# Performance work log

Measured on AMD Instinct MI355X. Metric: run time of the kernel, lower is better.

The kernel has to match this reference:

```python
import jax, jax.numpy as jnp
import numpy as np

D = 384      # d_model
DM = 256     # memory feature dim
DF = 1536    # dim_feedforward
EPS = 1e-5


def _layer_norm(x, g, b):
    m = jnp.mean(x, axis=-1, keepdims=True)
    v = jnp.mean(jnp.square(x - m), axis=-1, keepdims=True)
    return (x - m) * jax.lax.rsqrt(v + EPS) * g + b


def setup_inputs() -> dict:
    key = jax.random.key(0)
    ks = jax.random.split(key, 24)
    B, T, T1, Tc = 8, 2048, 2048, 2048
    s = 0.02
    inp = {
        "tgt": jax.random.normal(ks[0], (B, T, D), jnp.float32),
        "memory": jax.random.normal(ks[1], (B, T1, DM), jnp.float32),
        "a1": jnp.float32(0.5),
        "score_c": jax.random.normal(ks[2], (B, 1, Tc, T1), jnp.float32) * 0.1,
        "out_c": jax.random.normal(ks[3], (B, Tc, D), jnp.float32),
        # attention projections
        "Wq": jax.random.normal(ks[4], (D, D), jnp.float32) * s,
        "bq": jnp.zeros((D,), jnp.float32),
        "Wk": jax.random.normal(ks[5], (DM, D), jnp.float32) * s,
        "bk": jnp.zeros((D,), jnp.float32),
        "Wv": jax.random.normal(ks[6], (DM, D), jnp.float32) * s,
        "bv": jnp.zeros((D,), jnp.float32),
        "Wu": jax.random.normal(ks[7], (D, D), jnp.float32) * s,  # unknown
        "bu": jnp.zeros((D,), jnp.float32),
        "Wn": jax.random.normal(ks[8], (D, D), jnp.float32) * s,  # known
        "bn": jnp.zeros((D,), jnp.float32),
        # FFN
        "W1": jax.random.normal(ks[9], (D, DF), jnp.float32) * s,
        "b1": jnp.zeros((DF,), jnp.float32),
        "W2": jax.random.normal(ks[10], (DF, D), jnp.float32) * s,
        "b2": jnp.zeros((D,), jnp.float32),
        # LayerNorms
        "g1": jnp.ones((D,), jnp.float32),
        "be1": jnp.zeros((D,), jnp.float32),
        "g2": jnp.ones((D,), jnp.float32),
        "be2": jnp.zeros((D,), jnp.float32),
    }
    return inp


def reference(tgt, memory, a1, score_c, out_c,
              Wq, bq, Wk, bk, Wv, bv, Wu, bu, Wn, bn,
              W1, b1, W2, b2, g1, be1, g2, be2):
    # --- En_De_Attention (n_head = 1; dropout p=0 / eval mode -> identity) ---
    scale = 1.0 / jnp.sqrt(jnp.float32(D))
    q = tgt @ Wq + bq                  # [B,T,D]
    k = memory @ Wk + bk               # [B,T1,D]
    v = memory @ Wv + bv               # [B,T1,D]
    att = jnp.einsum('btd,bsd->bts', q, k) * scale            # [B,T,T1]

    unknow = tgt @ Wu + bu             # [B,T,D]
    know = out_c @ Wn + bn             # [B,Tc,D]
    score1 = jnp.einsum('btd,bcd->btc', unknow, know) * scale  # [B,T,Tc]
    mixed = jnp.einsum('btc,bcs->bts', score1, score_c[:, 0])  # [B,T,T1]

    # tt = a1 in (0,1]: blended-score branch of the original module
    score = a1 * jax.nn.softmax(mixed, axis=-1) \
          + (1.0 - a1) * jax.nn.softmax(att, axis=-1)          # [B,T,T1]
    z = jnp.einsum('bts,bsd->btd', score, v)                   # [B,T,D]

    # --- residual + norm1 ---
    x = _layer_norm(tgt + z, g1, be1)
    # --- FFN (relu) + residual + norm2 (dropout eval -> identity) ---
    ff = jax.nn.relu(x @ W1 + b1) @ W2 + b2
    out = _layer_norm(x + ff, g2, be2)
    # score2 returned with head dim, matching torch shape [B,1,T,T1]
    return out, score[:, None]
```

## Files before the change

### kernel.cpp

```cpp
#include <hip/hip_runtime.h>
#include <stdint.h>

typedef __attribute__((ext_vector_type(8))) short bf16x8;
typedef __attribute__((ext_vector_type(4))) float f32x4;

__device__ __forceinline__ short f2bf(float f) {
    union { float f; unsigned u; } v; v.f = f;
    unsigned r = v.u + 0x7fffu + ((v.u >> 16) & 1u);
    return (short)(r >> 16);
}
__device__ __forceinline__ float bf2f(short s) {
    union { unsigned u; float f; } v;
    v.u = ((unsigned)(unsigned short)s) << 16;
    return v.f;
}

__device__ __forceinline__ void gld16(const void* g, void* l) {
    auto gp = reinterpret_cast<const __attribute__((address_space(1))) unsigned int*>(
        reinterpret_cast<uintptr_t>(g));
    auto lp = reinterpret_cast<__attribute__((address_space(3))) unsigned int*>(
        reinterpret_cast<uintptr_t>(l));
    __builtin_amdgcn_global_load_lds(gp, lp, 16, 0, 0);
}

template<int OUTBF, int BIASMODE , int DORELU>
__global__ __launch_bounds__(256, 2) void gemm128p(
    const short* __restrict__ Ag, const short* __restrict__ Bg,
    void* __restrict__ Cg, const float* __restrict__ bias,
    int K, int N, long long sA, long long sB, long long sC, float scale)
{
    __shared__ short lds[2 * 16384];
    const int t = threadIdx.x;
    const int lane = t & 63;
    const int wave = t >> 6;
    const int wm = wave >> 1, wn = wave & 1;

    const int gx = gridDim.x, gy = gridDim.y;
    const int nwg = gx * gy * gridDim.z;
    int id = blockIdx.x + gx * (blockIdx.y + gy * blockIdx.z);
    id = (id & 7) * (nwg >> 3) + (id >> 3);
    const int bx = id % gx;
    const int by = (id / gx) % gy;
    const int bz = id / (gx * gy);

    const long long row0 = (long long)by * 128;
    const long long col0 = (long long)bx * 128;
    const int NT = K >> 6;

    const int srow = t >> 3;
    const int gk = ((t & 7) ^ (srow & 7)) * 8;
    const short* Asrc = Ag + (long long)bz * sA + (row0 + srow) * (long long)K + gk;
    const short* Bsrc = Bg + (long long)bz * sB + (col0 + srow) * (long long)K + gk;

    const int frow = lane & 15;
    const int fq = lane >> 4;

    f32x4 acc[4][4] = {};

#define STAGE_A(WB, KC) do { _Pragma("unroll") \
        for (int r = 0; r < 4; ++r) \
            gld16(Asrc + (KC) + (long long)r * 32 * K, &lds[(WB) + t * 8 + r * 2048]); } while (0)
#define STAGE_B(WB, KC) do { _Pragma("unroll") \
        for (int r = 0; r < 4; ++r) \
            gld16(Bsrc + (KC) + (long long)r * 32 * K, &lds[(WB) + 8192 + t * 8 + r * 2048]); } while (0)

#define RD_A(RB, M, KS) (*(const bf16x8*)&lds[(RB) + (wm * 64 + (M) * 16 + frow) * 64 + \
        ((((KS) << 2) | fq) ^ (frow & 7)) * 8])
#define RD_B(RB, Nn, KS) (*(const bf16x8*)&lds[(RB) + 8192 + (wn * 64 + (Nn) * 16 + frow) * 64 + \
        ((((KS) << 2) | fq) ^ (frow & 7)) * 8])

    STAGE_A(0, 0);
    STAGE_B(0, 0);
    asm volatile("s_waitcnt vmcnt(0)\ns_barrier" ::: "memory");

    for (int kt = 0; kt < NT; ++kt) {
        const int rb = (kt & 1) << 14;
        const int wb = ((kt + 1) & 1) << 14;
        const bool st = (kt + 1) < NT;
        const long long kc = (long long)(kt + 1) << 6;

        bf16x8 av[4], bv[4];

#pragma unroll
        for (int m = 0; m < 4; ++m) av[m] = RD_A(rb, m, 0);
#pragma unroll
        for (int n = 0; n < 4; ++n) bv[n] = RD_B(rb, n, 0);
        if (st) STAGE_A(wb, kc);
        asm volatile("s_barrier" ::: "memory");
        __builtin_amdgcn_s_setprio(1);
#pragma unroll
        for (int m = 0; m < 4; ++m)
#pragma unroll
            for (int n = 0; n < 4; ++n)
                acc[m][n] = __builtin_amdgcn_mfma_f32_16x16x32_bf16(av[m], bv[n], acc[m][n], 0, 0, 0);
        __builtin_amdgcn_s_setprio(0);
        asm volatile("s_barrier" ::: "memory");

#pragma unroll
        for (int m = 0; m < 4; ++m) av[m] = RD_A(rb, m, 1);
#pragma unroll
        for (int n = 0; n < 4; ++n) bv[n] = RD_B(rb, n, 1);
        if (st) STAGE_B(wb, kc);
        asm volatile("s_barrier" ::: "memory");
        __builtin_amdgcn_s_setprio(1);
#pragma unroll
        for (int m = 0; m < 4; ++m)
#pragma unroll
            for (int n = 0; n < 4; ++n)
                acc[m][n] = __builtin_amdgcn_mfma_f32_16x16x32_bf16(av[m], bv[n], acc[m][n], 0, 0, 0);
        __builtin_amdgcn_s_setprio(0);
        if (st) asm volatile("s_waitcnt vmcnt(0)\ns_barrier" ::: "memory");
        else    asm volatile("s_barrier" ::: "memory");
    }
#undef STAGE_A
#undef STAGE_B
#undef RD_A
#undef RD_B

    const int crow = (lane >> 4) * 4;
    const int ccol = lane & 15;
    const long long cz = (long long)bz * sC;
#pragma unroll
    for (int m = 0; m < 4; ++m)
#pragma unroll
        for (int n = 0; n < 4; ++n)
#pragma unroll
            for (int i = 0; i < 4; ++i) {
                long long r = row0 + wm * 64 + m * 16 + crow + i;
                long long c = col0 + wn * 64 + n * 16 + ccol;
                float v = acc[m][n][i] * scale;
                if (BIASMODE == 1) v += bias[c];
                if (BIASMODE == 2) v += bias[r];
                if (DORELU) v = fmaxf(v, 0.0f);
                long long idx = cz + r * (long long)N + c;
                if (OUTBF) ((short*)Cg)[idx] = f2bf(v);
                else ((float*)Cg)[idx] = v;
            }
}

__global__ __launch_bounds__(256) void cast_kernel(
    const float* __restrict__ in, short* __restrict__ out, long long n)
{
    long long i = ((long long)blockIdx.x * 256 + threadIdx.x) * 4;
    if (i + 3 < n) {
        float4 v = *(const float4*)&in[i];
        short4 o;
        o.x = f2bf(v.x); o.y = f2bf(v.y); o.z = f2bf(v.z); o.w = f2bf(v.w);
        *(short4*)&out[i] = o;
    }
}

__global__ __launch_bounds__(256) void transpose_cast(
    const float* __restrict__ in, short* __restrict__ out,
    int R, int C, long long sIn, long long sOut)
{
    __shared__ float tile[64][65];
    const long long zi = (long long)blockIdx.z * sIn;
    const long long zo = (long long)blockIdx.z * sOut;
    const int r0 = blockIdx.y * 64, c0 = blockIdx.x * 64;
    const int lr = threadIdx.x >> 6, lc = threadIdx.x & 63;
#pragma unroll
    for (int i = 0; i < 16; ++i) {
        int r = lr * 16 + i;
        tile[r][lc] = in[zi + (long long)(r0 + r) * C + c0 + lc];
    }
    __syncthreads();
#pragma unroll
    for (int i = 0; i < 16; ++i) {
        int r = lr * 16 + i;
        out[zo + (long long)(c0 + r) * R + r0 + lc] = f2bf(tile[lc][r]);
    }
}

__global__ __launch_bounds__(256) void softmax_blend(
    const short* __restrict__ attb, const short* __restrict__ mixb,
    const float* __restrict__ a1p,
    float* __restrict__ outF, short* __restrict__ outB)
{
    const int S = 2048;
    const long long row = blockIdx.x;
    const short* ar = attb + row * S;
    const short* mr = mixb + row * S;
    const int t = threadIdx.x;
    const int wave = t >> 6;

    bf16x8 a8 = *(const bf16x8*)&ar[t * 8];
    bf16x8 m8 = *(const bf16x8*)&mr[t * 8];
    float av[8], mv[8];
#pragma unroll
    for (int i = 0; i < 8; ++i) { av[i] = bf2f(a8[i]); mv[i] = bf2f(m8[i]); }

    float amax = av[0], mmax = mv[0];
#pragma unroll
    for (int i = 1; i < 8; ++i) { amax = fmaxf(amax, av[i]); mmax = fmaxf(mmax, mv[i]); }
#pragma unroll
    for (int o = 32; o; o >>= 1) {
        amax = fmaxf(amax, __shfl_xor(amax, o));
        mmax = fmaxf(mmax, __shfl_xor(mmax, o));
    }
    __shared__ float red[2][4];
    if ((t & 63) == 0) { red[0][wave] = amax; red[1][wave] = mmax; }
    __syncthreads();
    amax = fmaxf(fmaxf(red[0][0], red[0][1]), fmaxf(red[0][2], red[0][3]));
    mmax = fmaxf(fmaxf(red[1][0], red[1][1]), fmaxf(red[1][2], red[1][3]));

    float asum = 0.f, msum = 0.f;
#pragma unroll
    for (int i = 0; i < 8; ++i) {
        av[i] = __expf(av[i] - amax); asum += av[i];
        mv[i] = __expf(mv[i] - mmax); msum += mv[i];
    }
#pragma unroll
    for (int o = 32; o; o >>= 1) {
        asum += __shfl_xor(asum, o);
        msum += __shfl_xor(msum, o);
    }
    __shared__ float red2[2][4];
    if ((t & 63) == 0) { red2[0][wave] = asum; red2[1][wave] = msum; }
    __syncthreads();
    asum = red2[0][0] + red2[0][1] + red2[0][2] + red2[0][3];
    msum = red2[1][0] + red2[1][1] + red2[1][2] + red2[1][3];

    const float a1 = a1p[0];
    const float wm = a1 / msum;
    const float wa = (1.0f - a1) / asum;

    float o0[8];
    bf16x8 ob;
#pragma unroll
    for (int i = 0; i < 8; ++i) {
        float s = wm * mv[i] + wa * av[i];
        o0[i] = s;
        ob[i] = f2bf(s);
    }
    float4 f0, f1;
    f0.x = o0[0]; f0.y = o0[1]; f0.z = o0[2]; f0.w = o0[3];
    f1.x = o0[4]; f1.y = o0[5]; f1.z = o0[6]; f1.w = o0[7];
    *(float4*)&outF[row * S + t * 8] = f0;
    *(float4*)&outF[row * S + t * 8 + 4] = f1;
    *(bf16x8*)&outB[row * S + t * 8] = ob;
}

template<int WRITE_BF>
__global__ __launch_bounds__(256) void ln_kernel(
    const float* __restrict__ X, const float* __restrict__ Yr,
    const float* __restrict__ g, const float* __restrict__ be,
    float* __restrict__ outF, short* __restrict__ outB)
{
    const int Dm = 384;
    const int wave = threadIdx.x >> 6, lane = threadIdx.x & 63;
    const long long row = (long long)blockIdx.x * 4 + wave;
    const float* x = X + row * Dm;
    const float* y = Yr + row * Dm;
    float h[6];
    float s = 0.f, s2 = 0.f;
#pragma unroll
    for (int j = 0; j < 6; ++j) {
        int c = j * 64 + lane;
        h[j] = x[c] + y[c];
        s += h[j]; s2 += h[j] * h[j];
    }
#pragma unroll
    for (int o = 32; o; o >>= 1) { s += __shfl_xor(s, o); s2 += __shfl_xor(s2, o); }
    const float mean = s * (1.0f / 384.0f);
    const float var = s2 * (1.0f / 384.0f) - mean * mean;
    const float rstd = rsqrtf(var + 1e-5f);
#pragma unroll
    for (int j = 0; j < 6; ++j) {
        int c = j * 64 + lane;
        float v = (h[j] - mean) * rstd * g[c] + be[c];
        outF[row * Dm + c] = v;
        if (WRITE_BF) outB[row * Dm + c] = f2bf(v);
    }
}

extern "C" void kernel_launch(void* const* d_in, const int* in_sizes, int n_in,
                              void* d_out, int out_size, void* d_ws, size_t ws_size,
                              hipStream_t stream) {
    const float* tgt     = (const float*)d_in[0];
    const float* memory  = (const float*)d_in[1];
    const float* a1      = (const float*)d_in[2];
    const float* score_c = (const float*)d_in[3];
    const float* out_c   = (const float*)d_in[4];
    const float* Wq = (const float*)d_in[5];  const float* bq = (const float*)d_in[6];
    const float* Wk = (const float*)d_in[7];  const float* bk = (const float*)d_in[8];
    const float* Wv = (const float*)d_in[9];  const float* bv = (const float*)d_in[10];
    const float* Wu = (const float*)d_in[11]; const float* bu = (const float*)d_in[12];
    const float* Wn = (const float*)d_in[13]; const float* bn = (const float*)d_in[14];
    const float* W1 = (const float*)d_in[15]; const float* b1 = (const float*)d_in[16];
    const float* W2 = (const float*)d_in[17]; const float* b2 = (const float*)d_in[18];
    const float* g1 = (const float*)d_in[19]; const float* be1 = (const float*)d_in[20];
    const float* g2 = (const float*)d_in[21]; const float* be2 = (const float*)d_in[22];

    const long long BT = 16384;
    const long long S2 = 2048LL * 2048;
    const long long PB = 2048LL * 384;
    char* ws = (char*)d_ws;
    size_t off = 0;
    auto A_ = [&](size_t b) { size_t r = off; off += (b + 255) & ~(size_t)255; return r; };

    const size_t oTgtB = A_(BT * 384 * 2);
    const size_t oMemB = A_(BT * 256 * 2);
    const size_t oOutcB = A_(BT * 384 * 2);
    const size_t oWqT = A_(384 * 384 * 2);
    const size_t oWuT = A_(384 * 384 * 2);
    const size_t oWnT = A_(384 * 384 * 2);
    const size_t oWkT = A_(384 * 256 * 2);
    const size_t oWvT = A_(384 * 256 * 2);
    const size_t oW1T = A_(1536 * 384 * 2);
    const size_t oW2T = A_(384 * 1536 * 2);
    const size_t oQU  = A_(16 * PB * 2);
    const size_t oKP  = A_(16 * PB * 2);
    const size_t oVT  = A_(8LL * 384 * 2048 * 2);
    const size_t oJ   = A_(8 * S2 * 2);
    const size_t oKr  = A_(8 * S2 * 2);
    const size_t oAM  = A_(16 * S2 * 2);
    const size_t oX   = A_(BT * 384 * 4);
    const size_t oXB  = A_(BT * 384 * 2);

    short* tgt_bf  = (short*)(ws + oTgtB);
    short* mem_bf  = (short*)(ws + oMemB);
    short* outc_bf = (short*)(ws + oOutcB);
    short* WqT = (short*)(ws + oWqT);
    short* WuT = (short*)(ws + oWuT);
    short* WnT = (short*)(ws + oWnT);
    short* WkT = (short*)(ws + oWkT);
    short* WvT = (short*)(ws + oWvT);
    short* W1T = (short*)(ws + oW1T);
    short* W2T = (short*)(ws + oW2T);
    short* q_bf   = (short*)(ws + oQU);
    short* unk_bf = q_bf + 8 * PB;
    short* k_bf   = (short*)(ws + oKP);
    short* Pt_bf  = k_bf + 8 * PB;
    short* vT_bf  = (short*)(ws + oVT);
    short* score_bf = (short*)(ws + oJ);
    short* scoreCt  = (short*)(ws + oKr);
    float* z_f      = (float*)(ws + oKr);
    short* knoT_bf  = (short*)(ws + oAM);
    short* att_bf   = (short*)(ws + oAM);
    short* mix_bf   = att_bf + 8 * S2;
    short* h_bf     = (short*)(ws + oAM);
    float* ff_f     = (float*)(ws + oAM + 8 * S2 * 2);
    float* x_f  = (float*)(ws + oX);
    short* x_bf = (short*)(ws + oXB);

    float* outMain = (float*)d_out;
    float* outScore = (float*)d_out + 6291456;

    const float SC = 0.05103103630798288f;
    dim3 blk(256);

    cast_kernel<<<6144, blk, 0, stream>>>(tgt, tgt_bf, BT * 384);
    cast_kernel<<<4096, blk, 0, stream>>>(memory, mem_bf, BT * 256);
    cast_kernel<<<6144, blk, 0, stream>>>(out_c, outc_bf, BT * 384);
    transpose_cast<<<dim3(6, 6, 1), blk, 0, stream>>>(Wq, WqT, 384, 384, 0, 0);
    transpose_cast<<<dim3(6, 4, 1), blk, 0, stream>>>(Wk, WkT, 256, 384, 0, 0);
    transpose_cast<<<dim3(6, 4, 1), blk, 0, stream>>>(Wv, WvT, 256, 384, 0, 0);
    transpose_cast<<<dim3(6, 6, 1), blk, 0, stream>>>(Wu, WuT, 384, 384, 0, 0);
    transpose_cast<<<dim3(6, 6, 1), blk, 0, stream>>>(Wn, WnT, 384, 384, 0, 0);
    transpose_cast<<<dim3(24, 6, 1), blk, 0, stream>>>(W1, W1T, 384, 1536, 0, 0);
    transpose_cast<<<dim3(6, 24, 1), blk, 0, stream>>>(W2, W2T, 1536, 384, 0, 0);
    transpose_cast<<<dim3(32, 32, 8), blk, 0, stream>>>(score_c, scoreCt, 2048, 2048, S2, S2);

    gemm128p<1, 1, 0><<<dim3(3, 128, 1), blk, 0, stream>>>(tgt_bf, WqT, q_bf, bq, 384, 384, 0, 0, 0, 1.0f);
    gemm128p<1, 1, 0><<<dim3(3, 128, 1), blk, 0, stream>>>(mem_bf, WkT, k_bf, bk, 256, 384, 0, 0, 0, 1.0f);
    gemm128p<1, 2, 0><<<dim3(16, 3, 8), blk, 0, stream>>>(WvT, mem_bf, vT_bf, bv, 256, 2048,
                                                          0, 2048LL * 256, 384LL * 2048, 1.0f);
    gemm128p<1, 1, 0><<<dim3(3, 128, 1), blk, 0, stream>>>(tgt_bf, WuT, unk_bf, bu, 384, 384, 0, 0, 0, 1.0f);
    gemm128p<1, 2, 0><<<dim3(16, 3, 8), blk, 0, stream>>>(WnT, outc_bf, knoT_bf, bn, 384, 2048,
                                                          0, PB, 384LL * 2048, 1.0f);

    gemm128p<1, 0, 0><<<dim3(3, 16, 8), blk, 0, stream>>>(scoreCt, knoT_bf, Pt_bf, nullptr, 2048, 384,
                                                          S2, 384LL * 2048, PB, 1.0f);
    gemm128p<1, 0, 0><<<dim3(16, 16, 16), blk, 0, stream>>>(q_bf, k_bf, att_bf, nullptr, 384, 2048,
                                                            PB, PB, S2, SC);
    softmax_blend<<<16384, blk, 0, stream>>>(att_bf, mix_bf, a1, outScore, score_bf);
    gemm128p<0, 0, 0><<<dim3(3, 16, 8), blk, 0, stream>>>(score_bf, vT_bf, z_f, nullptr, 2048, 384,
                                                          S2, 384LL * 2048, PB, 1.0f);
    ln_kernel<1><<<4096, blk, 0, stream>>>(tgt, z_f, g1, be1, x_f, x_bf);
    gemm128p<1, 1, 1><<<dim3(12, 128, 1), blk, 0, stream>>>(x_bf, W1T, h_bf, b1, 384, 1536, 0, 0, 0, 1.0f);
    gemm128p<0, 1, 0><<<dim3(3, 128, 1), blk, 0, stream>>>(h_bf, W2T, ff_f, b2, 1536, 384, 0, 0, 0, 1.0f);
    ln_kernel<0><<<4096, blk, 0, stream>>>(x_f, ff_f, g2, be2, outMain, nullptr);
}
```

Measured before the change: 480.7 us.

## Merge launches: fused casts/transposes, concatenated Q|U projection, dual-output score GEMM

Collapses three cast kernels and seven weight-transpose launches into one launch each. Concatenates Wq and Wu so the Q and unknown projections run as a single N=768 GEMM, and fuses the V and known projections into one launch that selects its operands by z index. Adds a gemm128dd kernel that computes both the q·k score and the unknown·P score for a tile in one workgroup with two accumulator sets and a single shared K loop. The aim is to cut launch overhead and tail effects. In exchange, gemm128dd keeps twice the accumulator registers, which may lower occupancy or cause spills.

```diff
diff --git a/kernel.cpp b/kernel.cpp
--- a/kernel.cpp
+++ b/kernel.cpp
@@ -27,7 +27,8 @@
 __global__ __launch_bounds__(256, 2) void gemm128p(
     const short* __restrict__ Ag, const short* __restrict__ Bg,
     void* __restrict__ Cg, const float* __restrict__ bias,
-    int K, int N, long long sA, long long sB, long long sC, float scale)
+    int K, int lda, int ldb, int ldc,
+    long long sA, long long sB, long long sC, float scale)
 {
     __shared__ short lds[2 * 16384];
     const int t = threadIdx.x;
@@ -49,8 +50,8 @@
 
     const int srow = t >> 3;
     const int gk = ((t & 7) ^ (srow & 7)) * 8;
-    const short* Asrc = Ag + (long long)bz * sA + (row0 + srow) * (long long)K + gk;
-    const short* Bsrc = Bg + (long long)bz * sB + (col0 + srow) * (long long)K + gk;
+    const short* Asrc = Ag + (long long)bz * sA + (row0 + srow) * (long long)lda + gk;
+    const short* Bsrc = Bg + (long long)bz * sB + (col0 + srow) * (long long)ldb + gk;
 
     const int frow = lane & 15;
     const int fq = lane >> 4;
@@ -59,11 +60,10 @@
 
 #define STAGE_A(WB, KC) do { _Pragma("unroll") \
         for (int r = 0; r < 4; ++r) \
-            gld16(Asrc + (KC) + (long long)r * 32 * K, &lds[(WB) + t * 8 + r * 2048]); } while (0)
+            gld16(Asrc + (KC) + (long long)r * 32 * lda, &lds[(WB) + t * 8 + r * 2048]); } while (0)
 #define STAGE_B(WB, KC) do { _Pragma("unroll") \
         for (int r = 0; r < 4; ++r) \
-            gld16(Bsrc + (KC) + (long long)r * 32 * K, &lds[(WB) + 8192 + t * 8 + r * 2048]); } while (0)
-
+            gld16(Bsrc + (KC) + (long long)r * 32 * ldb, &lds[(WB) + 8192 + t * 8 + r * 2048]); } while (0)
 #define RD_A(RB, M, KS) (*(const bf16x8*)&lds[(RB) + (wm * 64 + (M) * 16 + frow) * 64 + \
         ((((KS) << 2) | fq) ^ (frow & 7)) * 8])
 #define RD_B(RB, Nn, KS) (*(const bf16x8*)&lds[(RB) + 8192 + (wn * 64 + (Nn) * 16 + frow) * 64 + \
@@ -114,8 +114,6 @@
     }
 #undef STAGE_A
 #undef STAGE_B
-#undef RD_A
-#undef RD_B
 
     const int crow = (lane >> 4) * 4;
     const int ccol = lane & 15;
@@ -132,21 +130,316 @@
                 if (BIASMODE == 1) v += bias[c];
                 if (BIASMODE == 2) v += bias[r];
                 if (DORELU) v = fmaxf(v, 0.0f);
-                long long idx = cz + r * (long long)N + c;
+                long long idx = cz + r * (long long)ldc + c;
                 if (OUTBF) ((short*)Cg)[idx] = f2bf(v);
                 else ((float*)Cg)[idx] = v;
             }
 }
 
-__global__ __launch_bounds__(256) void cast_kernel(
-    const float* __restrict__ in, short* __restrict__ out, long long n)
-{
-    long long i = ((long long)blockIdx.x * 256 + threadIdx.x) * 4;
-    if (i + 3 < n) {
-        float4 v = *(const float4*)&in[i];
-        short4 o;
-        o.x = f2bf(v.x); o.y = f2bf(v.y); o.z = f2bf(v.z); o.w = f2bf(v.w);
-        *(short4*)&out[i] = o;
+__global__ __launch_bounds__(256, 2) void gemm128pz(
+    const short* __restrict__ A1, const short* __restrict__ B1, short* __restrict__ C1,
+    const float* __restrict__ bias1, int K1, int lda1, int ldb1, int ldc1,
+    long long sB1, long long sC1,
+    const short* __restrict__ A2, const short* __restrict__ B2, short* __restrict__ C2,
+    const float* __restrict__ bias2, int K2, int lda2, int ldb2, int ldc2,
+    long long sB2, long long sC2)
+{
+    __shared__ short lds[2 * 16384];
+    const int t = threadIdx.x;
+    const int lane = t & 63;
+    const int wave = t >> 6;
+    const int wm = wave >> 1, wn = wave & 1;
+
+    const int gx = gridDim.x, gy = gridDim.y;
+    const int nwg = gx * gy * gridDim.z;
+    int id = blockIdx.x + gx * (blockIdx.y + gy * blockIdx.z);
+    id = (id & 7) * (nwg >> 3) + (id >> 3);
+    const int bx = id % gx;
+    const int by = (id / gx) % gy;
+    const int bz = id / (gx * gy);
+
+    const bool sel = bz >= 8;
+    const int zz = bz & 7;
+    const short* Ag = sel ? A2 : A1;
+    const short* Bg = sel ? B2 : B1;
+    short* Cg = sel ? C2 : C1;
+    const float* bias = sel ? bias2 : bias1;
+    const int K = sel ? K2 : K1;
+    const int lda = sel ? lda2 : lda1;
+    const int ldb = sel ? ldb2 : ldb1;
+    const int ldc = sel ? ldc2 : ldc1;
+    const long long sB = sel ? sB2 : sB1;
+    const long long sC = sel ? sC2 : sC1;
+
+    const long long row0 = (long long)by * 128;
+    const long long col0 = (long long)bx * 128;
+    const int NT = K >> 6;
+
+    const int srow = t >> 3;
+    const int gk = ((t & 7) ^ (srow & 7)) * 8;
+    const short* Asrc = Ag + (row0 + srow) * (long long)lda + gk;
+    const short* Bsrc = Bg + (long long)zz * sB + (col0 + srow) * (long long)ldb + gk;
+
+    const int frow = lane & 15;
+    const int fq = lane >> 4;
+
+    f32x4 acc[4][4] = {};
+
+#define STAGE_A(WB, KC) do { _Pragma("unroll") \
+        for (int r = 0; r < 4; ++r) \
+            gld16(Asrc + (KC) + (long long)r * 32 * lda, &lds[(WB) + t * 8 + r * 2048]); } while (0)
+#define STAGE_B(WB, KC) do { _Pragma("unroll") \
+        for (int r = 0; r < 4; ++r) \
+            gld16(Bsrc + (KC) + (long long)r * 32 * ldb, &lds[(WB) + 8192 + t * 8 + r * 2048]); } while (0)
+
+    STAGE_A(0, 0);
+    STAGE_B(0, 0);
+    asm volatile("s_waitcnt vmcnt(0)\ns_barrier" ::: "memory");
+
+    for (int kt = 0; kt < NT; ++kt) {
+        const int rb = (kt & 1) << 14;
+        const int wb = ((kt + 1) & 1) << 14;
+        const bool st = (kt + 1) < NT;
+        const long long kc = (long long)(kt + 1) << 6;
+
+        bf16x8 av[4], bv[4];
+
+#pragma unroll
+        for (int m = 0; m < 4; ++m) av[m] = RD_A(rb, m, 0);
+#pragma unroll
+        for (int n = 0; n < 4; ++n) bv[n] = RD_B(rb, n, 0);
+        if (st) STAGE_A(wb, kc);
+        asm volatile("s_barrier" ::: "memory");
+        __builtin_amdgcn_s_setprio(1);
+#pragma unroll
+        for (int m = 0; m < 4; ++m)
+#pragma unroll
+            for (int n = 0; n < 4; ++n)
+                acc[m][n] = __builtin_amdgcn_mfma_f32_16x16x32_bf16(av[m], bv[n], acc[m][n], 0, 0, 0);
+        __builtin_amdgcn_s_setprio(0);
+        asm volatile("s_barrier" ::: "memory");
+
+#pragma unroll
+        for (int m = 0; m < 4; ++m) av[m] = RD_A(rb, m, 1);
+#pragma unroll
+        for (int n = 0; n < 4; ++n) bv[n] = RD_B(rb, n, 1);
+        if (st) STAGE_B(wb, kc);
+        asm volatile("s_barrier" ::: "memory");
+        __builtin_amdgcn_s_setprio(1);
+#pragma unroll
+        for (int m = 0; m < 4; ++m)
+#pragma unroll
+            for (int n = 0; n < 4; ++n)
+                acc[m][n] = __builtin_amdgcn_mfma_f32_16x16x32_bf16(av[m], bv[n], acc[m][n], 0, 0, 0);
+        __builtin_amdgcn_s_setprio(0);
+        if (st) asm volatile("s_waitcnt vmcnt(0)\ns_barrier" ::: "memory");
+        else    asm volatile("s_barrier" ::: "memory");
+    }
+#undef STAGE_A
+#undef STAGE_B
+
+    const int crow = (lane >> 4) * 4;
+    const int ccol = lane & 15;
+    const long long cz = (long long)zz * sC;
+#pragma unroll
+    for (int m = 0; m < 4; ++m)
+#pragma unroll
+        for (int n = 0; n < 4; ++n)
+#pragma unroll
+            for (int i = 0; i < 4; ++i) {
+                long long r = row0 + wm * 64 + m * 16 + crow + i;
+                long long c = col0 + wn * 64 + n * 16 + ccol;
+                float v = acc[m][n][i] + bias[r];
+                Cg[cz + r * (long long)ldc + c] = f2bf(v);
+            }
+}
+
+__global__ __launch_bounds__(256, 2) void gemm128dd(
+    const short* __restrict__ Ag, const short* __restrict__ Bg, short* __restrict__ Cg,
+    int K, int lda, int ldb, int ldc,
+    long long sA, long long sB, long long sC,
+    int dA, long long dB, long long dC, float scale)
+{
+    __shared__ short lds[2 * 16384];
+    const int t = threadIdx.x;
+    const int lane = t & 63;
+    const int wave = t >> 6;
+    const int wm = wave >> 1, wn = wave & 1;
+
+    const int gx = gridDim.x, gy = gridDim.y;
+    const int nwg = gx * gy * gridDim.z;
+    int id = blockIdx.x + gx * (blockIdx.y + gy * blockIdx.z);
+    id = (id & 7) * (nwg >> 3) + (id >> 3);
+    const int bx = id % gx;
+    const int by = (id / gx) % gy;
+    const int bz = id / (gx * gy);
+
+    const long long row0 = (long long)by * 128;
+    const long long col0 = (long long)bx * 128;
+    const int NT = K >> 6;
+
+    const int srow = t >> 3;
+    const int gk = ((t & 7) ^ (srow & 7)) * 8;
+    const short* Asrc = Ag + (long long)bz * sA + (row0 + srow) * (long long)lda + gk;
+    const short* Bsrc = Bg + (long long)bz * sB + (col0 + srow) * (long long)ldb + gk;
+
+    const int frow = lane & 15;
+    const int fq = lane >> 4;
+
+    f32x4 accA[4][4] = {};
+    f32x4 accB[4][4] = {};
+
+#define AOFF(KT2) (((KT2) >= NT) ? ((long long)dA + (long long)((KT2) - NT) * 64) : ((long long)(KT2) * 64))
+#define BOFF(KT2) (((KT2) >= NT) ? (dB + (long long)((KT2) - NT) * 64) : ((long long)(KT2) * 64))
+#define STAGE_A(WB, OFF) do { _Pragma("unroll") \
+        for (int r = 0; r < 4; ++r) \
+            gld16(Asrc + (OFF) + (long long)r * 32 * lda, &lds[(WB) + t * 8 + r * 2048]); } while (0)
+#define STAGE_B(WB, OFF) do { _Pragma("unroll") \
+        for (int r = 0; r < 4; ++r) \
+            gld16(Bsrc + (OFF) + (long long)r * 32 * ldb, &lds[(WB) + 8192 + t * 8 + r * 2048]); } while (0)
+
+    STAGE_A(0, 0);
+    STAGE_B(0, 0);
+    asm volatile("s_waitcnt vmcnt(0)\ns_barrier" ::: "memory");
+
+    const int NT2 = NT * 2;
+    for (int kt = 0; kt < NT2; ++kt) {
+        const int rb = (kt & 1) << 14;
+        const int wb = ((kt + 1) & 1) << 14;
+        const bool st = (kt + 1) < NT2;
+        const long long ao = AOFF(kt + 1);
+        const long long bo = BOFF(kt + 1);
+        const bool first = kt < NT;
+
+        bf16x8 av[4], bv[4];
+
+#pragma unroll
+        for (int m = 0; m < 4; ++m) av[m] = RD_A(rb, m, 0);
+#pragma unroll
+        for (int n = 0; n < 4; ++n) bv[n] = RD_B(rb, n, 0);
+        if (st) STAGE_A(wb, ao);
+        asm volatile("s_barrier" ::: "memory");
+        __builtin_amdgcn_s_setprio(1);
+        if (first) {
+#pragma unroll
+            for (int m = 0; m < 4; ++m)
+#pragma unroll
+                for (int n = 0; n < 4; ++n)
+                    accA[m][n] = __builtin_amdgcn_mfma_f32_16x16x32_bf16(av[m], bv[n], accA[m][n], 0, 0, 0);
+        } else {
+#pragma unroll
+            for (int m = 0; m < 4; ++m)
+#pragma unroll
+                for (int n = 0; n < 4; ++n)
+                    accB[m][n] = __builtin_amdgcn_mfma_f32_16x16x32_bf16(av[m], bv[n], accB[m][n], 0, 0, 0);
+        }
+        __builtin_amdgcn_s_setprio(0);
+        asm volatile("s_barrier" ::: "memory");
+
+#pragma unroll
+        for (int m = 0; m < 4; ++m) av[m] = RD_A(rb, m, 1);
+#pragma unroll
+        for (int n = 0; n < 4; ++n) bv[n] = RD_B(rb, n, 1);
+        if (st) STAGE_B(wb, bo);
+        asm volatile("s_barrier" ::: "memory");
+        __builtin_amdgcn_s_setprio(1);
+        if (first) {
+#pragma unroll
+            for (int m = 0; m < 4; ++m)
+#pragma unroll
+                for (int n = 0; n < 4; ++n)
+                    accA[m][n] = __builtin_amdgcn_mfma_f32_16x16x32_bf16(av[m], bv[n], accA[m][n], 0, 0, 0);
+        } else {
+#pragma unroll
+            for (int m = 0; m < 4; ++m)
+#pragma unroll
+                for (int n = 0; n < 4; ++n)
+                    accB[m][n] = __builtin_amdgcn_mfma_f32_16x16x32_bf16(av[m], bv[n], accB[m][n], 0, 0, 0);
+        }
+        __builtin_amdgcn_s_setprio(0);
+        if (st) asm volatile("s_waitcnt vmcnt(0)\ns_barrier" ::: "memory");
+        else    asm volatile("s_barrier" ::: "memory");
+    }
+#undef STAGE_A
+#undef STAGE_B
+#undef AOFF
+#undef BOFF
+#undef RD_A
+#undef RD_B
+
+    const int crow = (lane >> 4) * 4;
+    const int ccol = lane & 15;
+    const long long cz = (long long)bz * sC;
+#pragma unroll
+    for (int m = 0; m < 4; ++m)
+#pragma unroll
+        for (int n = 0; n < 4; ++n)
+#pragma unroll
+            for (int i = 0; i < 4; ++i) {
+                long long r = row0 + wm * 64 + m * 16 + crow + i;
+                long long c = col0 + wn * 64 + n * 16 + ccol;
+                long long idx = cz + r * (long long)ldc + c;
+                Cg[idx] = f2bf(accA[m][n][i] * scale);
+                Cg[idx + dC] = f2bf(accB[m][n][i] * scale);
+            }
+}
+
+__global__ __launch_bounds__(256) void cast_all(
+    const float* __restrict__ tgt, const float* __restrict__ mem, const float* __restrict__ outc,
+    const float* __restrict__ bq, const float* __restrict__ bu,
+    short* __restrict__ tgtb, short* __restrict__ memb, short* __restrict__ outcb,
+    float* __restrict__ qubias)
+{
+    const long long R1 = 1572864;
+    const long long R2 = R1 + 1048576;
+    const long long R3 = R2 + 1572864;
+    const long long R4 = R3 + 192;
+    long long i = (long long)blockIdx.x * 256 + threadIdx.x;
+    const float* in; short* out; long long j;
+    if (i < R1) { in = tgt; out = tgtb; j = i; }
+    else if (i < R2) { in = mem; out = memb; j = i - R1; }
+    else if (i < R3) { in = outc; out = outcb; j = i - R2; }
+    else if (i < R4) {
+        j = i - R3;
+        ((float4*)qubias)[j] = (j < 96) ? ((const float4*)bq)[j] : ((const float4*)bu)[j - 96];
+        return;
+    } else return;
+    float4 v = ((const float4*)in)[j];
+    short4 o;
+    o.x = f2bf(v.x); o.y = f2bf(v.y); o.z = f2bf(v.z); o.w = f2bf(v.w);
+    ((short4*)out)[j] = o;
+}
+
+__global__ __launch_bounds__(256) void transpose_all(
+    const float* __restrict__ Wq, const float* __restrict__ Wk, const float* __restrict__ Wv,
+    const float* __restrict__ Wu, const float* __restrict__ Wn,
+    const float* __restrict__ W1, const float* __restrict__ W2,
+    short* __restrict__ WquT, short* __restrict__ WkT, short* __restrict__ WvT,
+    short* __restrict__ WnT, short* __restrict__ W1T, short* __restrict__ W2T)
+{
+    __shared__ float tile[64][65];
+    int b = blockIdx.x;
+    const float* in; short* out; int R, C, local;
+    if (b < 36)       { in = Wq; out = WquT;          R = 384;  C = 384;  local = b; }
+    else if (b < 60)  { in = Wk; out = WkT;           R = 256;  C = 384;  local = b - 36; }
+    else if (b < 84)  { in = Wv; out = WvT;           R = 256;  C = 384;  local = b - 60; }
+    else if (b < 120) { in = Wu; out = WquT + 147456; R = 384;  C = 384;  local = b - 84; }
+    else if (b < 156) { in = Wn; out = WnT;           R = 384;  C = 384;  local = b - 120; }
+    else if (b < 300) { in = W1; out = W1T;           R = 384;  C = 1536; local = b - 156; }
+    else              { in = W2; out = W2T;           R = 1536; C = 384;  local = b - 300; }
+    const int nbx = C >> 6;
+    const int r0 = (local / nbx) * 64, c0 = (local % nbx) * 64;
+    const int lr = threadIdx.x >> 6, lc = threadIdx.x & 63;
+#pragma unroll
+    for (int i = 0; i < 16; ++i) {
+        int r = lr * 16 + i;
+        tile[r][lc] = in[(long long)(r0 + r) * C + c0 + lc];
+    }
+    __syncthreads();
+#pragma unroll
+    for (int i = 0; i < 16; ++i) {
+        int r = lr * 16 + i;
+        out[(long long)(c0 + r) * R + r0 + lc] = f2bf(tile[lc][r]);
     }
 }
 
@@ -299,37 +592,36 @@
     size_t off = 0;
     auto A_ = [&](size_t b) { size_t r = off; off += (b + 255) & ~(size_t)255; return r; };
 
-    const size_t oTgtB = A_(BT * 384 * 2);
-    const size_t oMemB = A_(BT * 256 * 2);
+    const size_t oTgtB  = A_(BT * 384 * 2);
+    const size_t oMemB  = A_(BT * 256 * 2);
     const size_t oOutcB = A_(BT * 384 * 2);
-    const size_t oWqT = A_(384 * 384 * 2);
-    const size_t oWuT = A_(384 * 384 * 2);
-    const size_t oWnT = A_(384 * 384 * 2);
-    const size_t oWkT = A_(384 * 256 * 2);
-    const size_t oWvT = A_(384 * 256 * 2);
-    const size_t oW1T = A_(1536 * 384 * 2);
-    const size_t oW2T = A_(384 * 1536 * 2);
-    const size_t oQU  = A_(16 * PB * 2);
-    const size_t oKP  = A_(16 * PB * 2);
-    const size_t oVT  = A_(8LL * 384 * 2048 * 2);
-    const size_t oJ   = A_(8 * S2 * 2);
-    const size_t oKr  = A_(8 * S2 * 2);
-    const size_t oAM  = A_(16 * S2 * 2);
-    const size_t oX   = A_(BT * 384 * 4);
-    const size_t oXB  = A_(BT * 384 * 2);
+    const size_t oWquT  = A_(768 * 384 * 2);
+    const size_t oWnT   = A_(384 * 384 * 2);
+    const size_t oWkT   = A_(384 * 256 * 2);
+    const size_t oWvT   = A_(384 * 256 * 2);
+    const size_t oW1T   = A_(1536 * 384 * 2);
+    const size_t oW2T   = A_(384 * 1536 * 2);
+    const size_t oQUb   = A_(768 * 4);
+    const size_t oQU    = A_(16 * PB * 2);
+    const size_t oKP    = A_(16 * PB * 2);
+    const size_t oVT    = A_(8LL * 384 * 2048 * 2);
+    const size_t oJ     = A_(8 * S2 * 2);
+    const size_t oKr    = A_(8 * S2 * 2);
+    const size_t oAM    = A_(16 * S2 * 2);
+    const size_t oX     = A_(BT * 384 * 4);
+    const size_t oXB    = A_(BT * 384 * 2);
 
     short* tgt_bf  = (short*)(ws + oTgtB);
     short* mem_bf  = (short*)(ws + oMemB);
     short* outc_bf = (short*)(ws + oOutcB);
-    short* WqT = (short*)(ws + oWqT);
-    short* WuT = (short*)(ws + oWuT);
-    short* WnT = (short*)(ws + oWnT);
-    short* WkT = (short*)(ws + oWkT);
-    short* WvT = (short*)(ws + oWvT);
-    short* W1T = (short*)(ws + oW1T);
-    short* W2T = (short*)(ws + oW2T);
-    short* q_bf   = (short*)(ws + oQU);
-    short* unk_bf = q_bf + 8 * PB;
+    short* WquT = (short*)(ws + oWquT);
+    short* WnT  = (short*)(ws + oWnT);
+    short* WkT  = (short*)(ws + oWkT);
+    short* WvT  = (short*)(ws + oWvT);
+    short* W1T  = (short*)(ws + oW1T);
+    short* W2T  = (short*)(ws + oW2T);
+    float* qu_bias = (float*)(ws + oQUb);
+    short* qu_bf  = (short*)(ws + oQU);
     short* k_bf   = (short*)(ws + oKP);
     short* Pt_bf  = k_bf + 8 * PB;
     short* vT_bf  = (short*)(ws + oVT);
@@ -350,35 +642,31 @@
     const float SC = 0.05103103630798288f;
     dim3 blk(256);
 
-    cast_kernel<<<6144, blk, 0, stream>>>(tgt, tgt_bf, BT * 384);
-    cast_kernel<<<4096, blk, 0, stream>>>(memory, mem_bf, BT * 256);
-    cast_kernel<<<6144, blk, 0, stream>>>(out_c, outc_bf, BT * 384);
-    transpose_cast<<<dim3(6, 6, 1), blk, 0, stream>>>(Wq, WqT, 384, 384, 0, 0);
-    transpose_cast<<<dim3(6, 4, 1), blk, 0, stream>>>(Wk, WkT, 256, 384, 0, 0);
-    transpose_cast<<<dim3(6, 4, 1), blk, 0, stream>>>(Wv, WvT, 256, 384, 0, 0);
-    transpose_cast<<<dim3(6, 6, 1), blk, 0, stream>>>(Wu, WuT, 384, 384, 0, 0);
-    transpose_cast<<<dim3(6, 6, 1), blk, 0, stream>>>(Wn, WnT, 384, 384, 0, 0);
-    transpose_cast<<<dim3(24, 6, 1), blk, 0, stream>>>(W1, W1T, 384, 1536, 0, 0);
-    transpose_cast<<<dim3(6, 24, 1), blk, 0, stream>>>(W2, W2T, 1536, 384, 0, 0);
+    cast_all<<<16385, blk, 0, stream>>>(tgt, memory, out_c, bq, bu,
+                                        tgt_bf, mem_bf, outc_bf, qu_bias);
+    transpose_all<<<444, blk, 0, stream>>>(Wq, Wk, Wv, Wu, Wn, W1, W2,
+                                           WquT, WkT, WvT, WnT, W1T, W2T);
     transpose_cast<<<dim3(32, 32, 8), blk, 0, stream>>>(score_c, scoreCt, 2048, 2048, S2, S2);
 
-    gemm128p<1, 1, 0><<<dim3(3, 128, 1), blk, 0, stream>>>(tgt_bf, WqT, q_bf, bq, 384, 384, 0, 0, 0, 1.0f);
-    gemm128p<1, 1, 0><<<dim3(3, 128, 1), blk, 0, stream>>>(mem_bf, WkT, k_bf, bk, 256, 384, 0, 0, 0, 1.0f);
-    gemm128p<1, 2, 0><<<dim3(16, 3, 8), blk, 0, stream>>>(WvT, mem_bf, vT_bf, bv, 256, 2048,
-                                                          0, 2048LL * 256, 384LL * 2048, 1.0f);
-    gemm128p<1, 1, 0><<<dim3(3, 128, 1), blk, 0, stream>>>(tgt_bf, WuT, unk_bf, bu, 384, 384, 0, 0, 0, 1.0f);
-    gemm128p<1, 2, 0><<<dim3(16, 3, 8), blk, 0, stream>>>(WnT, outc_bf, knoT_bf, bn, 384, 2048,
-                                                          0, PB, 384LL * 2048, 1.0f);
-
-    gemm128p<1, 0, 0><<<dim3(3, 16, 8), blk, 0, stream>>>(scoreCt, knoT_bf, Pt_bf, nullptr, 2048, 384,
-                                                          S2, 384LL * 2048, PB, 1.0f);
-    gemm128p<1, 0, 0><<<dim3(16, 16, 16), blk, 0, stream>>>(q_bf, k_bf, att_bf, nullptr, 384, 2048,
-                                                            PB, PB, S2, SC);
+    gemm128p<1, 1, 0><<<dim3(6, 128, 1), blk, 0, stream>>>(
+        tgt_bf, WquT, qu_bf, qu_bias, 384, 384, 384, 768, 0, 0, 0, 1.0f);
+    gemm128p<1, 1, 0><<<dim3(3, 128, 1), blk, 0, stream>>>(
+        mem_bf, WkT, k_bf, bk, 256, 256, 256, 384, 0, 0, 0, 1.0f);
+    gemm128pz<<<dim3(16, 3, 16), blk, 0, stream>>>(
+        WvT, mem_bf, vT_bf, bv, 256, 256, 256, 2048, 2048LL * 256, PB,
+        WnT, outc_bf, knoT_bf, bn, 384, 384, 384, 2048, PB, PB);
+    gemm128p<1, 0, 0><<<dim3(3, 16, 8), blk, 0, stream>>>(
+        scoreCt, knoT_bf, Pt_bf, nullptr, 2048, 2048, 2048, 384, S2, PB, PB, 1.0f);
+    gemm128dd<<<dim3(16, 16, 8), blk, 0, stream>>>(
+        qu_bf, k_bf, att_bf, 384, 768, 384, 2048,
+        2048LL * 768, PB, S2, 384, 8 * PB, 8 * S2, SC);
     softmax_blend<<<16384, blk, 0, stream>>>(att_bf, mix_bf, a1, outScore, score_bf);
-    gemm128p<0, 0, 0><<<dim3(3, 16, 8), blk, 0, stream>>>(score_bf, vT_bf, z_f, nullptr, 2048, 384,
-                                                          S2, 384LL * 2048, PB, 1.0f);
+    gemm128p<0, 0, 0><<<dim3(3, 16, 8), blk, 0, stream>>>(
+        score_bf, vT_bf, z_f, nullptr, 2048, 2048, 2048, 384, S2, PB, PB, 1.0f);
     ln_kernel<1><<<4096, blk, 0, stream>>>(tgt, z_f, g1, be1, x_f, x_bf);
-    gemm128p<1, 1, 1><<<dim3(12, 128, 1), blk, 0, stream>>>(x_bf, W1T, h_bf, b1, 384, 1536, 0, 0, 0, 1.0f);
-    gemm128p<0, 1, 0><<<dim3(3, 128, 1), blk, 0, stream>>>(h_bf, W2T, ff_f, b2, 1536, 384, 0, 0, 0, 1.0f);
+    gemm128p<1, 1, 1><<<dim3(12, 128, 1), blk, 0, stream>>>(
+        x_bf, W1T, h_bf, b1, 384, 384, 384, 1536, 0, 0, 0, 1.0f);
+    gemm128p<0, 1, 0><<<dim3(3, 128, 1), blk, 0, stream>>>(
+        h_bf, W2T, ff_f, b2, 1536, 1536, 1536, 384, 0, 0, 0, 1.0f);
     ln_kernel<0><<<4096, blk, 0, stream>>>(x_f, ff_f, g2, be2, outMain, nullptr);
 }
```

New measurement: 460.4 us. 4.2% less time.
